# Kernel tuning notes

Measured on AMD Instinct MI355X. Metric: run time of the kernel, lower is better.

Reference implementation:

```python
import jax, jax.numpy as jnp
import numpy as np

B, N, H, NH, G, L, F = 64, 200, 256, 8, 2, 3, 512
Dh = H // NH


def _ln(x, sb):
    m = x.mean(-1, keepdims=True)
    v = x.var(-1, keepdims=True)
    return (x - m) / jnp.sqrt(v + 1e-5) * sb[0] + sb[1]


def setup_inputs() -> dict:
    key = jax.random.key(0)
    ks = jax.random.split(key, 24)
    rn = lambda k, sh, sc: jax.random.normal(k, sh, jnp.float32) * sc
    s = 1.0 / np.sqrt(H)
    ln_unit = jnp.stack([jnp.ones(H, jnp.float32), jnp.zeros(H, jnp.float32)])
    return {
        "enc_inputs": rn(ks[0], (B, N, H), 1.0),
        "dec_input": rn(ks[1], (B, H), 1.0),
        "dec_h": rn(ks[2], (B, H), 1.0),
        "dec_c": rn(ks[3], (B, H), 1.0),
        "gat_W": rn(ks[4], (G, H, NH * H), s),
        "gat_att_src": rn(ks[5], (G, NH, H), s),
        "gat_att_dst": rn(ks[6], (G, NH, H), s),
        "gat_bias": jnp.zeros((G, H), jnp.float32),
        "gat_ln": ln_unit,
        "enc_attn_W": rn(ks[7], (L, 4, H, H), s),
        "enc_attn_b": jnp.zeros((L, 4, H), jnp.float32),
        "enc_ln1": jnp.broadcast_to(ln_unit, (L, 2, H)),
        "enc_ffn_W1": rn(ks[8], (L, H, F), s),
        "enc_ffn_b1": jnp.zeros((L, F), jnp.float32),
        "enc_ffn_W2": rn(ks[9], (L, F, H), 1.0 / np.sqrt(F)),
        "enc_ffn_b2": jnp.zeros((L, H), jnp.float32),
        "enc_ln2": jnp.broadcast_to(ln_unit, (L, 2, H)),
        "lstm_Wih": rn(ks[10], (4 * H, H), s),
        "lstm_Whh": rn(ks[11], (4 * H, H), s),
        "lstm_b": jnp.zeros((4 * H,), jnp.float32),
        "ptr_Wref": rn(ks[12], (H, H), s),
        "ptr_Wq": rn(ks[13], (H, H), s),
        "ptr_v": rn(ks[14], (H,), s),
        "adj_mask": jax.random.randint(ks[15], (B, N, N), 0, 2, jnp.int32),
        "mask": jax.random.randint(ks[16], (B, N), 0, 2, jnp.int32),
    }


def _forward(enc_inputs, dec_input, dec_h, dec_c, gat_W, gat_att_src, gat_att_dst,
             gat_bias, gat_ln, enc_attn_W, enc_attn_b, enc_ln1, enc_ffn_W1,
             enc_ffn_b1, enc_ffn_W2, enc_ffn_b2, enc_ln2, lstm_Wih, lstm_Whh,
             lstm_b, ptr_Wref, ptr_Wq, ptr_v, adj_mask, mask):
    neg = jnp.float32(-1e9)
    # --- GAT stack (dense masked form of PyG GATConv; edges adj[i,j]: i->j, self-loops added) ---
    eye = jnp.eye(N, dtype=bool)
    A = jnp.where(eye[None], True, adj_mask > 0)  # [B,N,N] src i, tgt j
    Am = jnp.swapaxes(A, 1, 2)[..., None]  # [B, tgt j, src i, 1]
    x = enc_inputs
    for g in range(G):
        xp = (x @ gat_W[g]).reshape(B, N, NH, H)  # per-head transformed feats
        a_src = jnp.einsum('bnhd,hd->bnh', xp, gat_att_src[g])
        a_dst = jnp.einsum('bnhd,hd->bnh', xp, gat_att_dst[g])
        logit = jax.nn.leaky_relu(a_dst[:, :, None, :] + a_src[:, None, :, :], 0.2)
        logit = jnp.where(Am, logit, neg)  # [B,j,i,NH]
        attn = jax.nn.softmax(logit, axis=2)  # softmax over sources i per target j
        msg = jnp.einsum('bjih,bihd->bjhd', attn, xp).mean(axis=2) + gat_bias[g]
        x = x + jax.nn.relu(msg)  # residual per GAT layer
    emb = _ln(enc_inputs + jax.nn.relu(x), gat_ln)
    # --- Transformer encoder layers (masked self-attention, post-LN) ---
    amask = (adj_mask > 0)[:, None]  # [B,1,q,k]
    for l in range(L):
        q = (emb @ enc_attn_W[l, 0] + enc_attn_b[l, 0]).reshape(B, N, NH, Dh)
        k = (emb @ enc_attn_W[l, 1] + enc_attn_b[l, 1]).reshape(B, N, NH, Dh)
        v = (emb @ enc_attn_W[l, 2] + enc_attn_b[l, 2]).reshape(B, N, NH, Dh)
        sc = jnp.einsum('bqhd,bkhd->bhqk', q, k) / np.sqrt(Dh).astype(np.float32)
        sc = jnp.where(amask, sc, neg)
        at = jax.nn.softmax(sc, axis=-1)
        ctx = jnp.einsum('bhqk,bkhd->bqhd', at, v).reshape(B, N, H)
        emb = _ln(emb + ctx @ enc_attn_W[l, 3] + enc_attn_b[l, 3], enc_ln1[l])
        ff = jax.nn.relu(emb @ enc_ffn_W1[l] + enc_ffn_b1[l]) @ enc_ffn_W2[l] + enc_ffn_b2[l]
        emb = _ln(emb + ff, enc_ln2[l])
    # --- LSTM-cell pointer decoder ---
    gates = dec_input @ lstm_Wih.T + dec_h @ lstm_Whh.T + lstm_b
    i_g, f_g, g_g, o_g = jnp.split(gates, 4, axis=-1)
    c = jax.nn.sigmoid(f_g) * dec_c + jax.nn.sigmoid(i_g) * jnp.tanh(g_g)
    h = jax.nn.sigmoid(o_g) * jnp.tanh(c)
    u = jnp.tanh(emb @ ptr_Wref + (h @ ptr_Wq)[:, None, :]) @ ptr_v  # [B,N]
    u = jnp.where(mask > 0, u, neg)
    policy = jax.nn.softmax(u, axis=-1)
    return policy, h, c, emb


def reference(enc_inputs, dec_input, dec_h, dec_c, gat_W, gat_att_src, gat_att_dst,
              gat_bias, gat_ln, enc_attn_W, enc_attn_b, enc_ln1, enc_ffn_W1,
              enc_ffn_b1, enc_ffn_W2, enc_ffn_b2, enc_ln2, lstm_Wih, lstm_Whh,
              lstm_b, ptr_Wref, ptr_Wq, ptr_v, adj_mask, mask):
    return _forward(enc_inputs, dec_input, dec_h, dec_c, gat_W, gat_att_src,
                    gat_att_dst, gat_bias, gat_ln, enc_attn_W, enc_attn_b,
                    enc_ln1, enc_ffn_W1, enc_ffn_b1, enc_ffn_W2, enc_ffn_b2,
                    enc_ln2, lstm_Wih, lstm_Whh, lstm_b, ptr_Wref, ptr_Wq,
                    ptr_v, adj_mask, mask)
```

## Files before the change

### kernel.cpp

```cpp
#include <hip/hip_runtime.h>
#include <cstdio>
#include <math.h>

static constexpr int B_ = 64, N_ = 200, H_ = 256, NH_ = 8, G_ = 2, L_ = 3, F_ = 512;
static constexpr int BN_ = B_ * N_;

typedef unsigned short u16;
typedef __attribute__((ext_vector_type(8))) short short8;
typedef __attribute__((ext_vector_type(4))) float f32x4;

#define LDSP(p) ((__attribute__((address_space(3))) unsigned int*)(p))
#define GLBP(p) ((const __attribute__((address_space(1))) unsigned int*)(p))

__device__ __forceinline__ float wave_sum64(float v) {
#pragma unroll
  for (int off = 32; off; off >>= 1) v += __shfl_xor(v, off);
  return v;
}
__device__ __forceinline__ float sigmoidf_(float x) { return 1.f / (1.f + __expf(-x)); }
__device__ __forceinline__ u16 f2bf(float x) {
  unsigned u = __float_as_uint(x);
  return (u16)((u + 0x7FFFu + ((u >> 16) & 1u)) >> 16);
}
__device__ __forceinline__ float bf2f(u16 x) { return __uint_as_float((unsigned)x << 16); }

template <int ACT, bool HAS_BIAS, bool HAS_RES, bool OUT_BF>
__global__ __launch_bounds__(256) void gemm_bf16(
    const u16* __restrict__ A, const u16* __restrict__ Bt,
    const float* __restrict__ bias, const float* __restrict__ res,
    float* __restrict__ Cf, u16* __restrict__ Cb, int M, int Nn, int K) {
  __shared__ u16 As[128 * 64];
  __shared__ u16 Bs[128 * 64];
  char* asB = (char*)As;
  char* bsB = (char*)Bs;
  const int tid = threadIdx.x;
  const int m0 = blockIdx.x * 128, n0 = blockIdx.y * 128;
  const int lane = tid & 63;
  const int wid = tid >> 6;
  const int wr = (wid >> 1) * 64, wc = (wid & 1) * 64;
  const int Kb = K * 2;
  const char* Ab = (const char*)A + (size_t)m0 * Kb;
  const char* Bb = (const char*)Bt + (size_t)n0 * Kb;
  f32x4 acc[4][4];
#pragma unroll
  for (int i = 0; i < 4; ++i)
#pragma unroll
    for (int j = 0; j < 4; ++j)
#pragma unroll
      for (int r = 0; r < 4; ++r) acc[i][j][r] = 0.f;

  for (int k0 = 0; k0 < K; k0 += 64) {
    if (k0) __syncthreads();
#pragma unroll
    for (int it = 0; it < 4; ++it) {
      const unsigned o = (unsigned)(it * 256 + tid) * 16;
      const int row = o >> 7;
      const unsigned bc = (o & 127u) ^ (unsigned)((row & 7) << 4);
      const unsigned wb = o & ~1023u;
      __builtin_amdgcn_global_load_lds(GLBP(Ab + (size_t)row * Kb + k0 * 2 + bc),
                                       LDSP(asB + wb), 16, 0, 0);
      __builtin_amdgcn_global_load_lds(GLBP(Bb + (size_t)row * Kb + k0 * 2 + bc),
                                       LDSP(bsB + wb), 16, 0, 0);
    }
    __syncthreads();
#pragma unroll
    for (int kk = 0; kk < 2; ++kk) {
      short8 aF[4], bF[4];
#pragma unroll
      for (int i = 0; i < 4; ++i) {
        const int ar = wr + i * 16 + (lane & 15);
        const unsigned ac = (unsigned)(kk * 64 + (lane >> 4) * 16) ^ (unsigned)((ar & 7) << 4);
        aF[i] = *(const short8*)(asB + ar * 128 + ac);
        const int br = wc + i * 16 + (lane & 15);
        const unsigned bc2 = (unsigned)(kk * 64 + (lane >> 4) * 16) ^ (unsigned)((br & 7) << 4);
        bF[i] = *(const short8*)(bsB + br * 128 + bc2);
      }
#pragma unroll
      for (int i = 0; i < 4; ++i)
#pragma unroll
        for (int j = 0; j < 4; ++j)
          acc[i][j] = __builtin_amdgcn_mfma_f32_16x16x32_bf16(aF[i], bF[j], acc[i][j], 0, 0, 0);
    }
  }
#pragma unroll
  for (int i = 0; i < 4; ++i) {
    const int gm0 = m0 + wr + i * 16 + (lane >> 4) * 4;
#pragma unroll
    for (int j = 0; j < 4; ++j) {
      const int gn = n0 + wc + j * 16 + (lane & 15);
      const float bv = HAS_BIAS ? bias[gn] : 0.f;
#pragma unroll
      for (int r = 0; r < 4; ++r) {
        const int gm = gm0 + r;
        float v = acc[i][j][r] + bv;
        if (HAS_RES) v += res[(size_t)gm * Nn + gn];
        if (ACT == 1) v = fmaxf(v, 0.f);
        if (OUT_BF)
          Cb[(size_t)gm * Nn + gn] = f2bf(v);
        else
          Cf[(size_t)gm * Nn + gn] = v;
      }
    }
  }
}

template <int K>
__global__ __launch_bounds__(256) void gemm_ln(
    const u16* __restrict__ A, const u16* __restrict__ Bt,
    const float* __restrict__ bias, const float* __restrict__ res,
    const float* __restrict__ sb, float* __restrict__ out, u16* __restrict__ outB) {
  __shared__ u16 As[2][64 * 64];
  __shared__ u16 Bs[2][256 * 64];
  __shared__ float2 red[64][4];
  const int tid = threadIdx.x;
  const int m0 = blockIdx.x * 64;
  const int lane = tid & 63, wid = tid >> 6;
  const int wc = wid * 64;
  const int Kb = K * 2;
  const char* Ab = (const char*)A + (size_t)m0 * Kb;
  const char* Bb = (const char*)Bt;
  constexpr int T = K / 64;
  f32x4 acc[4][4];
#pragma unroll
  for (int i = 0; i < 4; ++i)
#pragma unroll
    for (int j = 0; j < 4; ++j)
#pragma unroll
      for (int r = 0; r < 4; ++r) acc[i][j][r] = 0.f;

  auto stage = [&](int buf, int k0) {
#pragma unroll
    for (int it = 0; it < 2; ++it) {
      const unsigned o = (unsigned)(it * 256 + tid) * 16;
      const int row = o >> 7;
      const unsigned bc = (o & 127u) ^ (unsigned)((row & 7) << 4);
      const unsigned wb = o & ~1023u;
      __builtin_amdgcn_global_load_lds(GLBP(Ab + (size_t)row * Kb + k0 * 2 + bc),
                                       LDSP((char*)As[buf] + wb), 16, 0, 0);
    }
#pragma unroll
    for (int it = 0; it < 8; ++it) {
      const unsigned o = (unsigned)(it * 256 + tid) * 16;
      const int row = o >> 7;
      const unsigned bc = (o & 127u) ^ (unsigned)((row & 7) << 4);
      const unsigned wb = o & ~1023u;
      __builtin_amdgcn_global_load_lds(GLBP(Bb + (size_t)row * Kb + k0 * 2 + bc),
                                       LDSP((char*)Bs[buf] + wb), 16, 0, 0);
    }
  };

  stage(0, 0);
  stage(1, 64);
  asm volatile("s_waitcnt vmcnt(10)" ::: "memory");
  __builtin_amdgcn_s_barrier();

  for (int t = 0; t < T; ++t) {
    const int cur = t & 1;
    const char* asB = (const char*)As[cur];
    const char* bsB = (const char*)Bs[cur];
#pragma unroll
    for (int kk = 0; kk < 2; ++kk) {
      short8 aF[4], bF[4];
#pragma unroll
      for (int i = 0; i < 4; ++i) {
        const int ar = i * 16 + (lane & 15);
        const unsigned ac = (unsigned)(kk * 64 + (lane >> 4) * 16) ^ (unsigned)((ar & 7) << 4);
        aF[i] = *(const short8*)(asB + ar * 128 + ac);
        const int br = wc + i * 16 + (lane & 15);
        const unsigned bc2 = (unsigned)(kk * 64 + (lane >> 4) * 16) ^ (unsigned)((br & 7) << 4);
        bF[i] = *(const short8*)(bsB + br * 128 + bc2);
      }
#pragma unroll
      for (int i = 0; i < 4; ++i)
#pragma unroll
        for (int j = 0; j < 4; ++j)
          acc[i][j] = __builtin_amdgcn_mfma_f32_16x16x32_bf16(aF[i], bF[j], acc[i][j], 0, 0, 0);
    }
    asm volatile("s_waitcnt lgkmcnt(0)" ::: "memory");
    __builtin_amdgcn_s_barrier();
    if (t + 2 < T) {
      stage(cur, (t + 2) * 64);
      asm volatile("s_waitcnt vmcnt(10)" ::: "memory");
      __builtin_amdgcn_s_barrier();
    } else if (t + 1 < T) {
      asm volatile("s_waitcnt vmcnt(0)" ::: "memory");
      __builtin_amdgcn_s_barrier();
    }
  }
#pragma unroll
  for (int i = 0; i < 4; ++i) {
#pragma unroll
    for (int j = 0; j < 4; ++j) {
      const int gn = wc + j * 16 + (lane & 15);
      const float bv = bias[gn];
#pragma unroll
      for (int r = 0; r < 4; ++r) {
        const int gm = m0 + i * 16 + (lane >> 4) * 4 + r;
        acc[i][j][r] += bv + res[(size_t)gm * 256 + gn];
      }
    }
  }
#pragma unroll
  for (int i = 0; i < 4; ++i) {
#pragma unroll
    for (int r = 0; r < 4; ++r) {
      float s = 0.f, q = 0.f;
#pragma unroll
      for (int j = 0; j < 4; ++j) {
        const float v = acc[i][j][r];
        s += v;
        q += v * v;
      }
#pragma unroll
      for (int off = 1; off < 16; off <<= 1) {
        s += __shfl_xor(s, off);
        q += __shfl_xor(q, off);
      }
      if ((lane & 15) == 0) red[i * 16 + (lane >> 4) * 4 + r][wid] = make_float2(s, q);
    }
  }
  __syncthreads();
#pragma unroll
  for (int i = 0; i < 4; ++i) {
#pragma unroll
    for (int r = 0; r < 4; ++r) {
      const int row = i * 16 + (lane >> 4) * 4 + r;
      const float2 p0 = red[row][0], p1 = red[row][1], p2 = red[row][2], p3 = red[row][3];
      const float S = p0.x + p1.x + p2.x + p3.x;
      const float Q = p0.y + p1.y + p2.y + p3.y;
      const float mean = S * (1.f / 256.f);
      const float var = Q * (1.f / 256.f) - mean * mean;
      const float rstd = rsqrtf(var + 1e-5f);
      const int gm = m0 + row;
#pragma unroll
      for (int j = 0; j < 4; ++j) {
        const int gn = wc + j * 16 + (lane & 15);
        const float y = (acc[i][j][r] - mean) * rstd * sb[gn] + sb[256 + gn];
        out[(size_t)gm * 256 + gn] = y;
        outB[(size_t)gm * 256 + gn] = f2bf(y);
      }
    }
  }
}

__global__ __launch_bounds__(256) void gat_projT(
    const u16* __restrict__ Wt, const u16* __restrict__ actB, u16* __restrict__ xpT) {
  __shared__ u16 As[128 * 64];
  __shared__ u16 Bs[128 * 64];
  char* asB = (char*)As;
  char* bsB = (char*)Bs;
  const int tid = threadIdx.x;
  const int m0 = blockIdx.x * 128;
  const int n0 = blockIdx.y * 128;
  const int b = blockIdx.z;
  const int lane = tid & 63;
  const int wid = tid >> 6;
  const int wr = (wid >> 1) * 64, wc = (wid & 1) * 64;
  const char* Ab = (const char*)Wt + (size_t)m0 * 512;
  const char* Bb = (const char*)actB + ((size_t)b * 200 + n0) * 512;
  f32x4 acc[4][4];
#pragma unroll
  for (int i = 0; i < 4; ++i)
#pragma unroll
    for (int j = 0; j < 4; ++j)
#pragma unroll
      for (int r = 0; r < 4; ++r) acc[i][j][r] = 0.f;

  for (int k0 = 0; k0 < 256; k0 += 64) {
    if (k0) __syncthreads();
#pragma unroll
    for (int it = 0; it < 4; ++it) {
      const unsigned o = (unsigned)(it * 256 + tid) * 16;
      const int row = o >> 7;
      const unsigned bc = (o & 127u) ^ (unsigned)((row & 7) << 4);
      const unsigned wb = o & ~1023u;
      __builtin_amdgcn_global_load_lds(GLBP(Ab + (size_t)row * 512 + k0 * 2 + bc),
                                       LDSP(asB + wb), 16, 0, 0);
      __builtin_amdgcn_global_load_lds(GLBP(Bb + (size_t)row * 512 + k0 * 2 + bc),
                                       LDSP(bsB + wb), 16, 0, 0);
    }
    __syncthreads();
#pragma unroll
    for (int kk = 0; kk < 2; ++kk) {
      short8 aF[4], bF[4];
#pragma unroll
      for (int i = 0; i < 4; ++i) {
        const int ar = wr + i * 16 + (lane & 15);
        const unsigned ac = (unsigned)(kk * 64 + (lane >> 4) * 16) ^ (unsigned)((ar & 7) << 4);
        aF[i] = *(const short8*)(asB + ar * 128 + ac);
        const int br = wc + i * 16 + (lane & 15);
        const unsigned bc2 = (unsigned)(kk * 64 + (lane >> 4) * 16) ^ (unsigned)((br & 7) << 4);
        bF[i] = *(const short8*)(bsB + br * 128 + bc2);
      }
#pragma unroll
      for (int i = 0; i < 4; ++i)
#pragma unroll
        for (int j = 0; j < 4; ++j)
          acc[i][j] = __builtin_amdgcn_mfma_f32_16x16x32_bf16(aF[i], bF[j], acc[i][j], 0, 0, 0);
    }
  }
  u16* outb = xpT + (size_t)b * 524288;
#pragma unroll
  for (int i = 0; i < 4; ++i) {
    const int gm0 = m0 + wr + i * 16 + (lane >> 4) * 4;
#pragma unroll
    for (int j = 0; j < 4; ++j) {
      const int gn = n0 + wc + j * 16 + (lane & 15);
#pragma unroll
      for (int r = 0; r < 4; ++r) {
        const int gm = gm0 + r;
        outb[(size_t)gm * 256 + gn] = (gn < N_) ? f2bf(acc[i][j][r]) : (u16)0;
      }
    }
  }
}

__global__ __launch_bounds__(256) void gat_msg_mfma(
    const u16* __restrict__ xpT, const float* __restrict__ asrcH,
    const float4* __restrict__ statsH, const unsigned* __restrict__ adjTW,
    const float* __restrict__ bias, const float* __restrict__ xin,
    float* __restrict__ xout, u16* __restrict__ xoutB) {
  __shared__ u16 Bs[2][256 * 64];
  __shared__ u16 Ps[2][32 * 64];
  const int tid = threadIdx.x;
  const int Lx = blockIdx.x;
  const int xcd = Lx & 7;
  const int slot = Lx >> 3;
  const int q = slot % 7;
  const int b = xcd + 8 * (slot / 7);
  const int m0 = q * 32;
  const int lane = tid & 63, wid = tid >> 6;
  const int wc = wid * 64;
  const char* baseB = (const char*)xpT + ((size_t)b << 20);
  f32x4 acc[2][4];
#pragma unroll
  for (int i = 0; i < 2; ++i)
#pragma unroll
    for (int j = 0; j < 4; ++j)
#pragma unroll
      for (int r = 0; r < 4; ++r) acc[i][j][r] = 0.f;

  auto stageB = [&](int buf, int t) {
    const size_t off = (size_t)(t >> 2) * 131072 + (size_t)((t & 3) * 128);
    char* bD = (char*)Bs[buf];
#pragma unroll
    for (int it = 0; it < 8; ++it) {
      const unsigned o = (unsigned)(it * 256 + tid) * 16;
      const int row = o >> 7;
      const unsigned bc = (o & 127u) ^ (unsigned)((row & 7) << 4);
      const unsigned wb = o & ~1023u;
      __builtin_amdgcn_global_load_lds(GLBP(baseB + off + (size_t)row * 512 + bc),
                                       LDSP(bD + wb), 16, 0, 0);
    }
  };
  auto computeP = [&](int buf, int t) {
    const int h = t >> 2, k0 = (t & 3) * 64;
    const size_t bh8 = ((size_t)(b * 8 + h)) << 8;
    const float* asp = asrcH + bh8 + k0;
    u16* P = Ps[buf];
    const int j = tid >> 3;
    const int ib = (tid & 7) << 3;
    const int gj = m0 + j;
    const int jc = gj < N_ ? gj : N_ - 1;
    const float4 st = statsH[bh8 + jc];
    const unsigned wbits =
        adjTW[((size_t)b * 256 + jc) * 8 + ((k0 + ib) >> 5)] >> ((k0 + ib) & 31);
    const float4 a0 = *(const float4*)(asp + ib);
    const float4 a1 = *(const float4*)(asp + ib + 4);
    const float av[8] = {a0.x, a0.y, a0.z, a0.w, a1.x, a1.y, a1.z, a1.w};
    float pv[8];
#pragma unroll
    for (int u = 0; u < 8; ++u) {
      float x = st.x + av[u];
      x = fmaxf(x, 0.2f * x);
      const float pe = __expf(x - st.y) * st.z;
      pv[u] = ((wbits >> u) & 1u) ? pe : 0.f;
    }
    unsigned pk[4];
#pragma unroll
    for (int qx = 0; qx < 4; ++qx)
      pk[qx] = (unsigned)f2bf(pv[2 * qx]) | ((unsigned)f2bf(pv[2 * qx + 1]) << 16);
    const unsigned ad2 =
        (unsigned)(j * 128) + (((unsigned)(ib * 2)) ^ (((unsigned)(j & 7)) << 4));
    *(uint4*)((char*)P + ad2) = make_uint4(pk[0], pk[1], pk[2], pk[3]);
  };

  stageB(0, 0);
  stageB(1, 1);
  computeP(0, 0);
  asm volatile("s_waitcnt lgkmcnt(0)" ::: "memory");
  asm volatile("s_waitcnt vmcnt(8)" ::: "memory");
  __builtin_amdgcn_s_barrier();

  for (int t = 0; t < 32; ++t) {
    const int cur = t & 1;
    if (t + 1 < 32) computeP(cur ^ 1, t + 1);
    const char* pB = (const char*)Ps[cur];
    const char* bB = (const char*)Bs[cur];
#pragma unroll
    for (int kk = 0; kk < 2; ++kk) {
      short8 aF[2], bF[4];
#pragma unroll
      for (int i = 0; i < 2; ++i) {
        const int ar = i * 16 + (lane & 15);
        const unsigned ac = (unsigned)(kk * 64 + (lane >> 4) * 16) ^ (unsigned)((ar & 7) << 4);
        aF[i] = *(const short8*)(pB + ar * 128 + ac);
      }
#pragma unroll
      for (int j = 0; j < 4; ++j) {
        const int br = wc + j * 16 + (lane & 15);
        const unsigned bc2 = (unsigned)(kk * 64 + (lane >> 4) * 16) ^ (unsigned)((br & 7) << 4);
        bF[j] = *(const short8*)(bB + br * 128 + bc2);
      }
#pragma unroll
      for (int i = 0; i < 2; ++i)
#pragma unroll
        for (int j = 0; j < 4; ++j)
          acc[i][j] = __builtin_amdgcn_mfma_f32_16x16x32_bf16(aF[i], bF[j], acc[i][j], 0, 0, 0);
    }
    asm volatile("s_waitcnt lgkmcnt(0)" ::: "memory");
    __builtin_amdgcn_s_barrier();
    if (t + 2 < 32) {
      stageB(cur, t + 2);
      asm volatile("s_waitcnt vmcnt(8)" ::: "memory");
      __builtin_amdgcn_s_barrier();
    } else if (t + 1 < 32) {
      asm volatile("s_waitcnt vmcnt(0)" ::: "memory");
      __builtin_amdgcn_s_barrier();
    }
  }
#pragma unroll
  for (int i = 0; i < 2; ++i) {
    const int gm0 = m0 + i * 16 + (lane >> 4) * 4;
#pragma unroll
    for (int j = 0; j < 4; ++j) {
      const int gn = wc + j * 16 + (lane & 15);
      const float bv = bias[gn];
#pragma unroll
      for (int r = 0; r < 4; ++r) {
        const int gm = gm0 + r;
        if (gm < N_) {
          const size_t oo = (size_t)(b * N_ + gm) * 256 + gn;
          const float v = xin[oo] + fmaxf(acc[i][j][r] * 0.125f + bv, 0.f);
          xout[oo] = v;
          xoutB[oo] = f2bf(v);
        }
      }
    }
  }
}

__global__ __launch_bounds__(256) void attn_fused(
    const u16* __restrict__ qkvB, const unsigned* __restrict__ adjW,
    u16* __restrict__ ctxB) {
  __shared__ __align__(16) u16 K_lds[208 * 40];
  __shared__ __align__(16) u16 V_lds[32 * 232];
  __shared__ __align__(16) u16 P_lds[4][16 * 232];
  const int Lx = blockIdx.x;
  const int b = (Lx & 7) + 8 * (Lx >> 6);
  const int h = (Lx >> 3) & 7;
  const int tid = threadIdx.x, lane = tid & 63, wid = tid >> 6;
  const u16* qb = qkvB + (size_t)b * 200 * 768;
  for (int e = tid; e < 200 * 32; e += 256) {
    const int kv = e >> 5, d = e & 31;
    K_lds[kv * 40 + d] = qb[(size_t)kv * 768 + 256 + h * 32 + d];
    V_lds[d * 232 + kv] = qb[(size_t)kv * 768 + 512 + h * 32 + d];
  }
  for (int e = tid; e < 32 * 24; e += 256) V_lds[(e / 24) * 232 + 200 + (e % 24)] = 0;
  const int g = lane >> 4, c = lane & 15;
  u16* Pw = P_lds[wid];
  for (int e = lane; e < 16 * 16; e += 64) Pw[(e >> 4) * 232 + 208 + (e & 15)] = 0;
  __syncthreads();
  short8 kf[13];
#pragma unroll
  for (int nt = 0; nt < 13; ++nt)
    kf[nt] = *(const short8*)&K_lds[(nt * 16 + c) * 40 + g * 8];
  const float scale = 0.17677669529663687f;
  for (int t = 0; t < 4; ++t) {
    const int m0 = (wid * 4 + t) * 16;
    int qrow = b * 200 + m0 + c;
    if (qrow > BN_ - 1) qrow = BN_ - 1;
    const short8 qf = *(const short8*)&qkvB[(size_t)qrow * 768 + h * 32 + g * 8];
    f32x4 acc[13];
#pragma unroll
    for (int nt = 0; nt < 13; ++nt) {
      f32x4 z = {0.f, 0.f, 0.f, 0.f};
      acc[nt] = __builtin_amdgcn_mfma_f32_16x16x32_bf16(qf, kf[nt], z, 0, 0, 0);
    }
    unsigned m8[4][8];
#pragma unroll
    for (int r = 0; r < 4; ++r) {
      const uint4* mp = (const uint4*)(adjW + ((size_t)b * 256 + m0 + g * 4 + r) * 8);
      const uint4 a0 = mp[0], a1 = mp[1];
      m8[r][0] = a0.x; m8[r][1] = a0.y; m8[r][2] = a0.z; m8[r][3] = a0.w;
      m8[r][4] = a1.x; m8[r][5] = a1.y; m8[r][6] = a1.z; m8[r][7] = a1.w;
    }
    float mx[4] = {-3e38f, -3e38f, -3e38f, -3e38f};
#pragma unroll
    for (int nt = 0; nt < 13; ++nt) {
      const int col = nt * 16 + c;
      const float sentinel = (col < 200) ? -1e9f : -2e9f;
#pragma unroll
      for (int r = 0; r < 4; ++r) {
        const bool ok = (m8[r][nt >> 1] >> (((nt & 1) << 4) + c)) & 1u;
        const float v = ok ? acc[nt][r] * scale : sentinel;
        acc[nt][r] = v;
        mx[r] = fmaxf(mx[r], v);
      }
    }
#pragma unroll
    for (int off = 1; off < 16; off <<= 1)
#pragma unroll
      for (int r = 0; r < 4; ++r) mx[r] = fmaxf(mx[r], __shfl_xor(mx[r], off));
    float sm[4] = {0.f, 0.f, 0.f, 0.f};
#pragma unroll
    for (int nt = 0; nt < 13; ++nt)
#pragma unroll
      for (int r = 0; r < 4; ++r) {
        const float e = __expf(acc[nt][r] - mx[r]);
        acc[nt][r] = e;
        sm[r] += e;
      }
#pragma unroll
    for (int off = 1; off < 16; off <<= 1)
#pragma unroll
      for (int r = 0; r < 4; ++r) sm[r] += __shfl_xor(sm[r], off);
#pragma unroll
    for (int r = 0; r < 4; ++r) sm[r] = 1.f / sm[r];
#pragma unroll
    for (int nt = 0; nt < 13; ++nt)
#pragma unroll
      for (int r = 0; r < 4; ++r)
        Pw[(g * 4 + r) * 232 + nt * 16 + c] = f2bf(acc[nt][r] * sm[r]);
    f32x4 o0 = {0.f, 0.f, 0.f, 0.f}, o1 = {0.f, 0.f, 0.f, 0.f};
#pragma unroll
    for (int kt = 0; kt < 7; ++kt) {
      const short8 pf = *(const short8*)&Pw[c * 232 + kt * 32 + g * 8];
      const short8 v0 = *(const short8*)&V_lds[c * 232 + kt * 32 + g * 8];
      const short8 v1 = *(const short8*)&V_lds[(16 + c) * 232 + kt * 32 + g * 8];
      o0 = __builtin_amdgcn_mfma_f32_16x16x32_bf16(pf, v0, o0, 0, 0, 0);
      o1 = __builtin_amdgcn_mfma_f32_16x16x32_bf16(pf, v1, o1, 0, 0, 0);
    }
#pragma unroll
    for (int r = 0; r < 4; ++r) {
      const int q = m0 + g * 4 + r;
      if (q < N_) {
        u16* od = ctxB + ((size_t)(b * N_ + q)) * 256 + h * 32;
        od[c] = f2bf(o0[r]);
        od[16 + c] = f2bf(o1[r]);
      }
    }
  }
}

__global__ __launch_bounds__(256) void adj_bits(const int* __restrict__ adj,
                                                unsigned* __restrict__ adjW) {
  const int b = blockIdx.x;
  for (int e = threadIdx.x; e < 256 * 8; e += 256) {
    const int row = e >> 3, w = e & 7;
    unsigned bits = 0u;
    if (row < N_ && w < 7) {
      const int base = w * 32;
      const int lim = (N_ - base) < 32 ? (N_ - base) : 32;
      const int* ar = adj + ((size_t)b * N_ + row) * N_ + base;
      for (int i = 0; i < lim; ++i) bits |= (ar[i] > 0 ? 1u : 0u) << i;
    }
    adjW[((size_t)b * 256 + row) * 8 + w] = bits;
  }
}

__global__ __launch_bounds__(256) void adj_bits2(const int* __restrict__ adjT,
                                                 unsigned* __restrict__ adjTW) {
  const int b = blockIdx.x;
  for (int e = threadIdx.x; e < 256 * 8; e += 256) {
    const int j = e >> 3, w = e & 7;
    unsigned bits = 0u;
    if (j < N_ && w < 7) {
      const int base = w * 32;
      const int lim = (N_ - base) < 32 ? (N_ - base) : 32;
      const int* ar = adjT + ((size_t)b * N_ + j) * N_ + base;
      for (int i = 0; i < lim; ++i) bits |= (ar[i] > 0 ? 1u : 0u) << i;
      if (j >= base && j < base + 32) bits |= 1u << (j - base);
    }
    adjTW[((size_t)b * 256 + j) * 8 + w] = bits;
  }
}

__global__ __launch_bounds__(256) void adj_transpose(const int* __restrict__ adj,
                                                     int* __restrict__ adjT) {
  __shared__ int s[32][33];
  const int b = blockIdx.z;
  const int i0 = blockIdx.x * 32, j0 = blockIdx.y * 32;
  const int tx = threadIdx.x & 31, ty = threadIdx.x >> 5;
#pragma unroll
  for (int u = 0; u < 4; ++u) {
    const int i = i0 + ty + 8 * u, j = j0 + tx;
    if (i < N_ && j < N_) s[ty + 8 * u][tx] = adj[((size_t)b * N_ + i) * N_ + j];
  }
  __syncthreads();
#pragma unroll
  for (int u = 0; u < 4; ++u) {
    const int j = j0 + ty + 8 * u, i = i0 + tx;
    if (i < N_ && j < N_) adjT[((size_t)b * N_ + j) * N_ + i] = s[tx][ty + 8 * u];
  }
}

__device__ const int PREP_TBL[21][6] = {
    {0, 0, 0, 0, 256, 2048},
    {0, 524288, 0, 524288, 256, 2048},
    {1, 0 * 65536, 1, 0, 256, 256},      {1, 1 * 65536, 1, 65536, 256, 256},
    {1, 2 * 65536, 1, 131072, 256, 256}, {1, 4 * 65536, 1, 196608, 256, 256},
    {1, 5 * 65536, 1, 262144, 256, 256}, {1, 6 * 65536, 1, 327680, 256, 256},
    {1, 8 * 65536, 1, 393216, 256, 256}, {1, 9 * 65536, 1, 458752, 256, 256},
    {1, 10 * 65536, 1, 524288, 256, 256},
    {1, 3 * 65536, 2, 0, 256, 256},      {1, 7 * 65536, 2, 65536, 256, 256},
    {1, 11 * 65536, 2, 131072, 256, 256},
    {2, 0, 3, 0, 256, 512}, {2, 131072, 3, 131072, 256, 512}, {2, 262144, 3, 262144, 256, 512},
    {3, 0, 4, 0, 512, 256}, {3, 131072, 4, 131072, 512, 256}, {3, 262144, 4, 262144, 512, 256},
    {4, 0, 5, 0, 256, 256},
};

__global__ __launch_bounds__(256) void prep_weights(
    const float* __restrict__ gat_W, const float* __restrict__ attn_W,
    const float* __restrict__ W1, const float* __restrict__ W2,
    const float* __restrict__ Wref, u16* __restrict__ gatWT, u16* __restrict__ WqkvT,
    u16* __restrict__ WoT, u16* __restrict__ W1T, u16* __restrict__ W2T,
    u16* __restrict__ WrefT) {
  const int mi = blockIdx.y;
  const int R = PREP_TBL[mi][4], C = PREP_TBL[mi][5];
  const int tc = C / 32;
  const int tiles = (R / 32) * tc;
  if ((int)blockIdx.x >= tiles) return;
  const int sel = PREP_TBL[mi][0], dsel = PREP_TBL[mi][2];
  const float* sp = (sel == 0) ? gat_W : (sel == 1) ? attn_W : (sel == 2) ? W1 : (sel == 3) ? W2 : Wref;
  u16* dp = (dsel == 0) ? gatWT : (dsel == 1) ? WqkvT : (dsel == 2) ? WoT : (dsel == 3) ? W1T
            : (dsel == 4) ? W2T : WrefT;
  sp += PREP_TBL[mi][1];
  dp += PREP_TBL[mi][3];
  const int r0 = (blockIdx.x / tc) * 32, c0 = (blockIdx.x % tc) * 32;
  __shared__ float s[32][33];
  const int tx = threadIdx.x & 31, ty = threadIdx.x >> 5;
#pragma unroll
  for (int u = 0; u < 4; ++u) s[ty + 8 * u][tx] = sp[(size_t)(r0 + ty + 8 * u) * C + c0 + tx];
  __syncthreads();
#pragma unroll
  for (int u = 0; u < 4; ++u)
    dp[(size_t)(c0 + ty + 8 * u) * R + r0 + tx] = f2bf(s[tx][ty + 8 * u]);
}

__global__ __launch_bounds__(256) void cast_bf16(const float* __restrict__ in,
                                                 u16* __restrict__ out, int n4) {
  const int i = blockIdx.x * 256 + threadIdx.x;
  if (i >= n4) return;
  const float4 v = ((const float4*)in)[i];
  ushort4 o;
  o.x = f2bf(v.x); o.y = f2bf(v.y); o.z = f2bf(v.z); o.w = f2bf(v.w);
  ((ushort4*)out)[i] = o;
}

__global__ __launch_bounds__(256) void gat_attvec_stats(
    const u16* __restrict__ xpT, const float* __restrict__ att_src,
    const float* __restrict__ att_dst, const unsigned* __restrict__ adjTW,
    float* __restrict__ asrcH, float4* __restrict__ statsH) {
  __shared__ float as_l[256];
  __shared__ float ad_l[256];
  const int bh = blockIdx.x;
  const int b = bh >> 3, h = bh & 7;
  const int i = threadIdx.x;
  const u16* base = xpT + (size_t)bh * 65536 + i;
  const float* vs = att_src + h * 256;
  const float* vd = att_dst + h * 256;
  float ps = 0.f, pd = 0.f;
  for (int d = 0; d < 256; ++d) {
    const float x = bf2f(base[(size_t)d * 256]);
    ps += x * vs[d];
    pd += x * vd[d];
  }
  as_l[i] = ps;
  ad_l[i] = pd;
  asrcH[bh * 256 + i] = ps;
  __syncthreads();
  const int j = i;
  if (j < N_) {
    unsigned wbits[7];
#pragma unroll
    for (int w = 0; w < 7; ++w) wbits[w] = adjTW[((size_t)b * 256 + j) * 8 + w];
    const float ad = ad_l[j];
    float mx = -1e30f;
#pragma unroll
    for (int w = 0; w < 7; ++w) {
      const unsigned bits = wbits[w];
      for (int t = 0; t < 32; ++t) {
        float x = ad + as_l[w * 32 + t];
        x = fmaxf(x, 0.2f * x);
        x = ((bits >> t) & 1u) ? x : -1e9f;
        mx = fmaxf(mx, x);
      }
    }
    float sum = 0.f;
#pragma unroll
    for (int w = 0; w < 7; ++w) {
      const unsigned bits = wbits[w];
      for (int t = 0; t < 32; ++t) {
        float x = ad + as_l[w * 32 + t];
        x = fmaxf(x, 0.2f * x);
        x = ((bits >> t) & 1u) ? x : -1e9f;
        sum += __expf(x - mx);
      }
    }
    statsH[(size_t)bh * 256 + j] = make_float4(ad, mx, 1.f / sum, 0.f);
  }
}

__global__ __launch_bounds__(256) void ln_pre_kernel(
    const float* __restrict__ in1, const float* __restrict__ in2,
    const float* __restrict__ sb, float* __restrict__ out, u16* __restrict__ outB) {
  const int row = blockIdx.x, t = threadIdx.x;
  const long o = (long)row * 256 + t;
  const float v = in1[o] + fmaxf(in2[o], 0.f);
  float s = v, q = v * v;
#pragma unroll
  for (int off = 32; off; off >>= 1) {
    s += __shfl_xor(s, off);
    q += __shfl_xor(q, off);
  }
  __shared__ float sh[8];
  const int wid = t >> 6, lane = t & 63;
  if (lane == 0) {
    sh[wid] = s;
    sh[4 + wid] = q;
  }
  __syncthreads();
  const float S = sh[0] + sh[1] + sh[2] + sh[3];
  const float Q = sh[4] + sh[5] + sh[6] + sh[7];
  const float mean = S * (1.f / 256.f);
  const float var = Q * (1.f / 256.f) - mean * mean;
  const float r = rsqrtf(var + 1e-5f);
  const float y = (v - mean) * r * sb[t] + sb[256 + t];
  out[o] = y;
  outB[o] = f2bf(y);
}

__global__ __launch_bounds__(256) void lstm_gates(
    const float* __restrict__ di, const float* __restrict__ dh,
    const float* __restrict__ Wih, const float* __restrict__ Whh,
    const float* __restrict__ bias, float* __restrict__ gates) {
  const int idx = blockIdx.x * 256 + threadIdx.x;
  const int b = idx >> 10, n = idx & 1023;
  const float4* w1 = (const float4*)(Wih + (size_t)n * 256);
  const float4* w2 = (const float4*)(Whh + (size_t)n * 256);
  const float4* x1 = (const float4*)(di + b * 256);
  const float4* x2 = (const float4*)(dh + b * 256);
  float s = bias[n];
  for (int k = 0; k < 64; ++k) {
    const float4 a = x1[k], wv = w1[k];
    const float4 a2 = x2[k], wv2 = w2[k];
    s += a.x * wv.x + a.y * wv.y + a.z * wv.z + a.w * wv.w;
    s += a2.x * wv2.x + a2.y * wv2.y + a2.z * wv2.z + a2.w * wv2.w;
  }
  gates[idx] = s;
}

__global__ __launch_bounds__(256) void lstm_ew(
    const float* __restrict__ gates, const float* __restrict__ dc,
    float* __restrict__ h_out, float* __restrict__ c_out) {
  const int idx = blockIdx.x * 256 + threadIdx.x;
  const int b = idx >> 8, d = idx & 255;
  const float ig = sigmoidf_(gates[b * 1024 + d]);
  const float fg = sigmoidf_(gates[b * 1024 + 256 + d]);
  const float gg = tanhf(gates[b * 1024 + 512 + d]);
  const float og = sigmoidf_(gates[b * 1024 + 768 + d]);
  const float c = fg * dc[idx] + ig * gg;
  c_out[idx] = c;
  h_out[idx] = og * tanhf(c);
}

__global__ __launch_bounds__(256) void hq_gemm(
    const float* __restrict__ h, const float* __restrict__ Wq, float* __restrict__ hq) {
  const int b = blockIdx.x;
  const int n = threadIdx.x;
  float s = 0.f;
  for (int k = 0; k < 256; ++k) s += h[b * 256 + k] * Wq[k * 256 + n];
  hq[b * 256 + n] = s;
}

__global__ __launch_bounds__(64) void ptr_u(
    const float* __restrict__ pref, const float* __restrict__ hq,
    const float* __restrict__ pv, float* __restrict__ u) {
  const int row = blockIdx.x;
  const int b = row / N_;
  const int lane = threadIdx.x;
  float s = 0.f;
  for (int d = lane; d < 256; d += 64)
    s += tanhf(pref[(long)row * 256 + d] + hq[b * 256 + d]) * pv[d];
  s = wave_sum64(s);
  if (lane == 0) u[row] = s;
}

__global__ __launch_bounds__(256) void policy_softmax(
    const float* __restrict__ u, const int* __restrict__ mask, float* __restrict__ pol) {
  const int b = blockIdx.x, t = threadIdx.x;
  float val = -1e30f;
  if (t < N_) val = (mask[b * N_ + t] > 0) ? u[b * N_ + t] : -1e9f;
  float m = val;
#pragma unroll
  for (int off = 32; off; off >>= 1) m = fmaxf(m, __shfl_xor(m, off));
  __shared__ float sh[8];
  const int wid = t >> 6, lane = t & 63;
  if (lane == 0) sh[wid] = m;
  __syncthreads();
  m = fmaxf(fmaxf(sh[0], sh[1]), fmaxf(sh[2], sh[3]));
  const float e = (t < N_) ? __expf(val - m) : 0.f;
  float s = e;
#pragma unroll
  for (int off = 32; off; off >>= 1) s += __shfl_xor(s, off);
  __syncthreads();
  if (lane == 0) sh[4 + wid] = s;
  __syncthreads();
  const float S = sh[4] + sh[5] + sh[6] + sh[7];
  if (t < N_) pol[b * N_ + t] = e / S;
}

extern "C" void kernel_launch(void* const* d_in, const int* in_sizes, int n_in,
                              void* d_out, int out_size, void* d_ws, size_t ws_size,
                              hipStream_t stream) {
  const float* enc_inputs = (const float*)d_in[0];
  const float* dec_input = (const float*)d_in[1];
  const float* dec_h = (const float*)d_in[2];
  const float* dec_c = (const float*)d_in[3];
  const float* gat_W = (const float*)d_in[4];
  const float* gat_att_src = (const float*)d_in[5];
  const float* gat_att_dst = (const float*)d_in[6];
  const float* gat_bias = (const float*)d_in[7];
  const float* gat_ln = (const float*)d_in[8];
  const float* enc_attn_W = (const float*)d_in[9];
  const float* enc_attn_b = (const float*)d_in[10];
  const float* enc_ln1 = (const float*)d_in[11];
  const float* enc_ffn_W1 = (const float*)d_in[12];
  const float* enc_ffn_b1 = (const float*)d_in[13];
  const float* enc_ffn_W2 = (const float*)d_in[14];
  const float* enc_ffn_b2 = (const float*)d_in[15];
  const float* enc_ln2 = (const float*)d_in[16];
  const float* lstm_Wih = (const float*)d_in[17];
  const float* lstm_Whh = (const float*)d_in[18];
  const float* lstm_b = (const float*)d_in[19];
  const float* ptr_Wref = (const float*)d_in[20];
  const float* ptr_Wq = (const float*)d_in[21];
  const float* ptr_v = (const float*)d_in[22];
  const int* adj = (const int*)d_in[23];
  const int* mask = (const int*)d_in[24];

  float* out = (float*)d_out;
  float* policy = out;
  float* h_out = out + 12800;
  float* c_out = out + 12800 + 16384;
  float* emb = out + 12800 + 16384 + 16384;

  char* ws = (char*)d_ws;
  char* arena = ws;
  size_t o = 134217728;
  float* xbuf = (float*)(ws + o); o += 13107200;
  float* gates = (float*)(ws + o); o += 262144;
  float* hq = (float*)(ws + o); o += 65536;
  float* ubuf = (float*)(ws + o); o += 51200;
  u16* encB = (u16*)(ws + o); o += 6553600;
  u16* xbufB = (u16*)(ws + o); o += 6553600;
  u16* embB = (u16*)(ws + o); o += 6553600;
  int* adjT = (int*)(ws + o); o += 10240000;
  unsigned* adjW = (unsigned*)(ws + o); o += 524288;
  unsigned* adjTW = (unsigned*)(ws + o); o += 524288;
  float* asrcH = (float*)(ws + o); o += 524288;
  float4* statsH = (float4*)(ws + o); o += 2097152;
  u16* gatWT = (u16*)(ws + o); o += 2097152;
  u16* WqkvT = (u16*)(ws + o); o += 1179648;
  u16* WoT = (u16*)(ws + o); o += 393216;
  u16* W1T = (u16*)(ws + o); o += 786432;
  u16* W2T = (u16*)(ws + o); o += 786432;
  u16* WrefT = (u16*)(ws + o); o += 131072;
  if (ws_size < o) fprintf(stderr, "kernel_launch: ws too small (%zu < %zu)\n", ws_size, o);
  u16* xpT = (u16*)arena;
  u16* qkvB = (u16*)arena;
  u16* ctxB = (u16*)(arena + 19660800);
  u16* ffnB = (u16*)(arena + 26214400);
  float* pref = (float*)arena;

  prep_weights<<<dim3(512, 21), 256, 0, stream>>>(gat_W, enc_attn_W, enc_ffn_W1, enc_ffn_W2,
                                                  ptr_Wref, gatWT, WqkvT, WoT, W1T, W2T, WrefT);
  cast_bf16<<<3200, 256, 0, stream>>>(enc_inputs, encB, 819200);
  adj_transpose<<<dim3(7, 7, 64), 256, 0, stream>>>(adj, adjT);
  adj_bits<<<64, 256, 0, stream>>>(adj, adjW);
  adj_bits2<<<64, 256, 0, stream>>>(adjT, adjTW);

  for (int g = 0; g < G_; ++g) {
    const u16* actB = (g == 0) ? encB : xbufB;
    const float* xin = (g == 0) ? enc_inputs : xbuf;
    gat_projT<<<dim3(16, 2, 64), 256, 0, stream>>>(gatWT + (size_t)g * 524288, actB, xpT);
    gat_attvec_stats<<<512, 256, 0, stream>>>(xpT, gat_att_src + g * 2048,
                                              gat_att_dst + g * 2048, adjTW, asrcH, statsH);
    gat_msg_mfma<<<448, 256, 0, stream>>>(xpT, asrcH, statsH, adjTW, gat_bias + g * H_,
                                          xin, xbuf, xbufB);
  }
  ln_pre_kernel<<<BN_, 256, 0, stream>>>(enc_inputs, xbuf, gat_ln, emb, embB);

  for (int l = 0; l < L_; ++l) {
    gemm_bf16<0, true, false, true><<<dim3(100, 6), 256, 0, stream>>>(
        embB, WqkvT + (size_t)l * 196608, enc_attn_b + l * 1024, nullptr, nullptr, qkvB,
        BN_, 768, 256);
    attn_fused<<<512, 256, 0, stream>>>(qkvB, adjW, ctxB);
    gemm_ln<256><<<200, 256, 0, stream>>>(ctxB, WoT + (size_t)l * 65536,
                                          enc_attn_b + l * 1024 + 768, emb,
                                          enc_ln1 + l * 512, emb, embB);
    gemm_bf16<1, true, false, true><<<dim3(100, 4), 256, 0, stream>>>(
        embB, W1T + (size_t)l * 131072, enc_ffn_b1 + l * 512, nullptr, nullptr, ffnB,
        BN_, 512, 256);
    gemm_ln<512><<<200, 256, 0, stream>>>(ffnB, W2T + (size_t)l * 131072,
                                          enc_ffn_b2 + l * 256, emb,
                                          enc_ln2 + l * 512, emb, embB);
  }

  lstm_gates<<<256, 256, 0, stream>>>(dec_input, dec_h, lstm_Wih, lstm_Whh, lstm_b, gates);
  lstm_ew<<<64, 256, 0, stream>>>(gates, dec_c, h_out, c_out);
  hq_gemm<<<64, 256, 0, stream>>>(h_out, ptr_Wq, hq);
  gemm_bf16<0, false, false, false><<<dim3(100, 2), 256, 0, stream>>>(
      embB, WrefT, nullptr, nullptr, pref, nullptr, BN_, 256, 256);
  ptr_u<<<BN_, 64, 0, stream>>>(pref, hq, ptr_v, ubuf);
  policy_softmax<<<B_, 256, 0, stream>>>(ubuf, mask, policy);
}
```

Before: 567.1 us.

## Double-buffer GEMM LDS tiles and vectorize GAT attention-vector reduction

The bf16 GEMM now keeps two LDS buffers and prefetches the K-tile two steps ahead with global_load_lds, using vmcnt waits and barriers to overlap loads with MFMA work. The GAT attention-vector kernel now has each thread load 8 bf16 values at once over a 32-deep slice of d, then reduces the partial sums across 8 groups in LDS, replacing the strided scalar loop. This doubles LDS use in the GEMM, which may lower occupancy. The hand-written waitcnt counts assume exactly 8 outstanding loads per stage, and the prologue assumes K is at least 128.

```diff
diff --git a/kernel.cpp b/kernel.cpp
--- a/kernel.cpp
+++ b/kernel.cpp
@@ -29,10 +29,8 @@
     const u16* __restrict__ A, const u16* __restrict__ Bt,
     const float* __restrict__ bias, const float* __restrict__ res,
     float* __restrict__ Cf, u16* __restrict__ Cb, int M, int Nn, int K) {
-  __shared__ u16 As[128 * 64];
-  __shared__ u16 Bs[128 * 64];
-  char* asB = (char*)As;
-  char* bsB = (char*)Bs;
+  __shared__ u16 As[2][128 * 64];
+  __shared__ u16 Bs[2][128 * 64];
   const int tid = threadIdx.x;
   const int m0 = blockIdx.x * 128, n0 = blockIdx.y * 128;
   const int lane = tid & 63;
@@ -41,6 +39,7 @@
   const int Kb = K * 2;
   const char* Ab = (const char*)A + (size_t)m0 * Kb;
   const char* Bb = (const char*)Bt + (size_t)n0 * Kb;
+  const int T = K >> 6;
   f32x4 acc[4][4];
 #pragma unroll
   for (int i = 0; i < 4; ++i)
@@ -49,8 +48,7 @@
 #pragma unroll
       for (int r = 0; r < 4; ++r) acc[i][j][r] = 0.f;
 
-  for (int k0 = 0; k0 < K; k0 += 64) {
-    if (k0) __syncthreads();
+  auto stage = [&](int buf, int k0) {
 #pragma unroll
     for (int it = 0; it < 4; ++it) {
       const unsigned o = (unsigned)(it * 256 + tid) * 16;
@@ -58,11 +56,21 @@
       const unsigned bc = (o & 127u) ^ (unsigned)((row & 7) << 4);
       const unsigned wb = o & ~1023u;
       __builtin_amdgcn_global_load_lds(GLBP(Ab + (size_t)row * Kb + k0 * 2 + bc),
-                                       LDSP(asB + wb), 16, 0, 0);
+                                       LDSP((char*)As[buf] + wb), 16, 0, 0);
       __builtin_amdgcn_global_load_lds(GLBP(Bb + (size_t)row * Kb + k0 * 2 + bc),
-                                       LDSP(bsB + wb), 16, 0, 0);
-    }
-    __syncthreads();
+                                       LDSP((char*)Bs[buf] + wb), 16, 0, 0);
+    }
+  };
+
+  stage(0, 0);
+  stage(1, 64);
+  asm volatile("s_waitcnt vmcnt(8)" ::: "memory");
+  __builtin_amdgcn_s_barrier();
+
+  for (int t = 0; t < T; ++t) {
+    const int cur = t & 1;
+    const char* asB = (const char*)As[cur];
+    const char* bsB = (const char*)Bs[cur];
 #pragma unroll
     for (int kk = 0; kk < 2; ++kk) {
       short8 aF[4], bF[4];
@@ -80,6 +88,16 @@
 #pragma unroll
         for (int j = 0; j < 4; ++j)
           acc[i][j] = __builtin_amdgcn_mfma_f32_16x16x32_bf16(aF[i], bF[j], acc[i][j], 0, 0, 0);
+    }
+    asm volatile("s_waitcnt lgkmcnt(0)" ::: "memory");
+    __builtin_amdgcn_s_barrier();
+    if (t + 2 < T) {
+      stage(cur, (t + 2) * 64);
+      asm volatile("s_waitcnt vmcnt(8)" ::: "memory");
+      __builtin_amdgcn_s_barrier();
+    } else if (t + 1 < T) {
+      asm volatile("s_waitcnt vmcnt(0)" ::: "memory");
+      __builtin_amdgcn_s_barrier();
     }
   }
 #pragma unroll
@@ -662,38 +680,60 @@
     const u16* __restrict__ xpT, const float* __restrict__ att_src,
     const float* __restrict__ att_dst, const unsigned* __restrict__ adjTW,
     float* __restrict__ asrcH, float4* __restrict__ statsH) {
+  __shared__ float pAs[8][256];
+  __shared__ float pAd[8][256];
   __shared__ float as_l[256];
   __shared__ float ad_l[256];
   const int bh = blockIdx.x;
   const int b = bh >> 3, h = bh & 7;
-  const int i = threadIdx.x;
-  const u16* base = xpT + (size_t)bh * 65536 + i;
-  const float* vs = att_src + h * 256;
-  const float* vd = att_dst + h * 256;
-  float ps = 0.f, pd = 0.f;
-  for (int d = 0; d < 256; ++d) {
-    const float x = bf2f(base[(size_t)d * 256]);
-    ps += x * vs[d];
-    pd += x * vd[d];
-  }
-  as_l[i] = ps;
-  ad_l[i] = pd;
-  asrcH[bh * 256 + i] = ps;
+  const int t = threadIdx.x;
+  const int ig = (t & 31) * 8;
+  const int dg = t >> 5;
+  const u16* base = xpT + (size_t)bh * 65536 + (size_t)(dg * 32) * 256 + ig;
+  const float* vs = att_src + h * 256 + dg * 32;
+  const float* vd = att_dst + h * 256 + dg * 32;
+  float ps[8] = {0.f, 0.f, 0.f, 0.f, 0.f, 0.f, 0.f, 0.f};
+  float pd[8] = {0.f, 0.f, 0.f, 0.f, 0.f, 0.f, 0.f, 0.f};
+  for (int dd = 0; dd < 32; ++dd) {
+    const short8 xv = *(const short8*)(base + (size_t)dd * 256);
+    const float wvs = vs[dd], wvd = vd[dd];
+#pragma unroll
+    for (int u = 0; u < 8; ++u) {
+      const float x = bf2f((u16)xv[u]);
+      ps[u] += x * wvs;
+      pd[u] += x * wvd;
+    }
+  }
+#pragma unroll
+  for (int u = 0; u < 8; ++u) {
+    pAs[dg][ig + u] = ps[u];
+    pAd[dg][ig + u] = pd[u];
+  }
   __syncthreads();
-  const int j = i;
+  float as = 0.f, ad = 0.f;
+#pragma unroll
+  for (int g2 = 0; g2 < 8; ++g2) {
+    as += pAs[g2][t];
+    ad += pAd[g2][t];
+  }
+  as_l[t] = as;
+  ad_l[t] = ad;
+  asrcH[bh * 256 + t] = as;
+  __syncthreads();
+  const int j = t;
   if (j < N_) {
     unsigned wbits[7];
 #pragma unroll
     for (int w = 0; w < 7; ++w) wbits[w] = adjTW[((size_t)b * 256 + j) * 8 + w];
-    const float ad = ad_l[j];
+    const float adv = ad_l[j];
     float mx = -1e30f;
 #pragma unroll
     for (int w = 0; w < 7; ++w) {
       const unsigned bits = wbits[w];
-      for (int t = 0; t < 32; ++t) {
-        float x = ad + as_l[w * 32 + t];
+      for (int tt = 0; tt < 32; ++tt) {
+        float x = adv + as_l[w * 32 + tt];
         x = fmaxf(x, 0.2f * x);
-        x = ((bits >> t) & 1u) ? x : -1e9f;
+        x = ((bits >> tt) & 1u) ? x : -1e9f;
         mx = fmaxf(mx, x);
       }
     }
@@ -701,14 +741,14 @@
 #pragma unroll
     for (int w = 0; w < 7; ++w) {
       const unsigned bits = wbits[w];
-      for (int t = 0; t < 32; ++t) {
-        float x = ad + as_l[w * 32 + t];
+      for (int tt = 0; tt < 32; ++tt) {
+        float x = adv + as_l[w * 32 + tt];
         x = fmaxf(x, 0.2f * x);
-        x = ((bits >> t) & 1u) ? x : -1e9f;
+        x = ((bits >> tt) & 1u) ? x : -1e9f;
         sum += __expf(x - mx);
       }
     }
-    statsH[(size_t)bh * 256 + j] = make_float4(ad, mx, 1.f / sum, 0.f);
+    statsH[(size_t)bh * 256 + j] = make_float4(adv, mx, 1.f / sum, 0.f);
   }
 }
 
```

Measured after the change: 571.4 us. About the same (+0.8%).
